# Optimization experiments

Measured on AMD Instinct MI355X. Metric: run time of the kernel, lower is better.

Reference implementation:

```python
import jax, jax.numpy as jnp
import numpy as np
from functools import partial

VOCAB = 1000
HID = 512
EPS = 1e-3  # Keras BatchNorm default epsilon


def _conv1d(x, w, stride):
    # x: [B,T,C_in], w: [K,C_in,C_out]
    return jax.lax.conv_general_dilated(x, w, window_strides=(stride,), padding='SAME',
                                        dimension_numbers=('NWC', 'WIO', 'NWC'))


def setup_inputs() -> dict:
    key = jax.random.key(0)
    ks = jax.random.split(key, 8)
    s = lambda *sh: 1.0 / np.sqrt(sh[-2] if len(sh) > 1 else sh[-1])
    return {
        'x': jax.random.normal(ks[0], (32, 1600, 80), jnp.float32),
        'y_true': jax.random.randint(ks[1], (32, 201), 0, VOCAB),
        'bn_gamma': jnp.ones((80,), jnp.float32),
        'bn_beta': jnp.zeros((80,), jnp.float32),
        'conv0_w': jax.random.normal(ks[2], (5, 80, 512), jnp.float32) * 0.05,
        'conv0_b': jnp.zeros((512,), jnp.float32),
        'tcr_w': jax.random.normal(ks[3], (4, 5, 512, 512), jnp.float32) * 0.02,
        'tcr_b': jnp.zeros((4, 512), jnp.float32),
        'gru_kernel': jax.random.normal(ks[4], (VOCAB, 3 * HID), jnp.float32) * 0.03,
        'gru_rec_kernel': jax.random.normal(ks[5], (HID, 3 * HID), jnp.float32) * 0.04,
        'gru_bias': jnp.zeros((2, 3 * HID), jnp.float32),
        'fc_w': jax.random.normal(ks[6], (2 * HID, VOCAB), jnp.float32) * 0.03,
        'fc_b': jnp.zeros((VOCAB,), jnp.float32),
    }


def reference(x, y_true, bn_gamma, bn_beta, conv0_w, conv0_b, tcr_w, tcr_b,
              gru_kernel, gru_rec_kernel, gru_bias, fc_w, fc_b):
    # ---- Encoder ----
    # BatchNorm (training mode: batch statistics over batch & time)
    mean = jnp.mean(x, axis=(0, 1))
    var = jnp.var(x, axis=(0, 1))
    h = (x - mean) * jax.lax.rsqrt(var + EPS) * bn_gamma + bn_beta
    # strided Conv1D + relu -> [B, T=800, 512]
    h = jax.nn.relu(_conv1d(h, conv0_w, 2) + conv0_b)
    # Temporal conv residual blocks: out = relu(conv(x)) + x
    for i in range(tcr_w.shape[0]):
        h = jax.nn.relu(_conv1d(h, tcr_w[i], 1) + tcr_b[i]) + h
    enc = h  # [B, T, D]
    B = enc.shape[0]

    # ---- Decoder (teacher forcing, training branch) ----
    y_oh = jax.nn.one_hot(y_true, VOCAB, dtype=jnp.float32)  # [B, U+1, V]
    inputs = jnp.transpose(y_oh[:, :-1, :], (1, 0, 2))       # [U, B, V]
    bi, br = gru_bias[0], gru_bias[1]

    def step(hstate, y_u):
        # Keras GRUCell (reset_after=True)
        mx = y_u @ gru_kernel + bi
        mh = hstate @ gru_rec_kernel + br
        xz, xr, xh = jnp.split(mx, 3, axis=-1)
        hz, hr, hh = jnp.split(mh, 3, axis=-1)
        z = jax.nn.sigmoid(xz + hz)
        r = jax.nn.sigmoid(xr + hr)
        cand = jnp.tanh(xh + r * hh)
        h_new = z * hstate + (1.0 - z) * cand
        # Dot-product attention over encoder states
        scores = jnp.einsum('bd,btd->bt', h_new, enc)
        alpha = jax.nn.softmax(scores, axis=-1)
        ctx = jnp.einsum('bt,btd->bd', alpha, enc)
        # output projection with softmax activation
        y_pred = jax.nn.softmax(jnp.concatenate([h_new, ctx], axis=1) @ fc_w + fc_b, axis=-1)
        return h_new, y_pred

    h0 = jnp.zeros((B, HID), jnp.float32)
    _, outs = jax.lax.scan(step, h0, inputs)  # [U, B, V]
    return jnp.transpose(outs, (1, 0, 2))     # [B, U, V]
```

## Files before the change

### kernel.cpp

```cpp
#include <hip/hip_runtime.h>
#include <cstdint>

typedef _Float16 f16;
typedef __attribute__((ext_vector_type(2))) _Float16 f16x2;
typedef __attribute__((ext_vector_type(8))) _Float16 f16x8;
typedef __attribute__((ext_vector_type(4))) float f32x4;
typedef __attribute__((ext_vector_type(2))) float f32x2;
typedef __attribute__((ext_vector_type(8))) unsigned short us8;
typedef __attribute__((ext_vector_type(4))) int i32x4;

#define NB   32
#define TIN  1600
#define CIN  80
#define TOUT 800
#define DH   512
#define NV   1000
#define NU   200
#define TXP  1604
#define THP  804
#define EPSB 1e-3f
#define EWG  248

__device__ __forceinline__ void st_sys_f16(f16* p, float v)
{
    f16 h = (f16)v;
    short s; __builtin_memcpy(&s, &h, 2);
    int si = (int)s;
    asm volatile("global_store_short %0, %1, off sc0 sc1"
                 :: "v"(p), "v"(si) : "memory");
}
__device__ __forceinline__ void st_sys_i32(int* p, int v)
{
    asm volatile("global_store_dword %0, %1, off sc0 sc1"
                 :: "v"(p), "v"(v) : "memory");
}

__device__ __forceinline__ void poll8(const int* fl, int target)
{
    i32x4 a, b;
    while (true) {
        asm volatile("global_load_dwordx4 %0, %2, off sc1\n\t"
                     "global_load_dwordx4 %1, %3, off sc1\n\t"
                     "s_waitcnt vmcnt(0)"
                     : "=&v"(a), "=&v"(b)
                     : "v"(fl), "v"(fl + 4)
                     : "memory");
        if (a.x == target && a.y == target && a.z == target && a.w == target &&
            b.x == target && b.y == target && b.z == target && b.w == target) break;
        __builtin_amdgcn_s_sleep(1);
    }
}

__device__ __forceinline__ float fast_tanh(float x)
{
    return 1.f - 2.f / (__expf(2.f * x) + 1.f);
}

__global__ void init_zero(float* gsum, float* gsumsq,
                          int* flags, int* lcnt, f16* xpad, f16* hbufA, f16* hbufB)
{
    int tid = blockIdx.x * 256 + threadIdx.x;
    int stride = gridDim.x * 256;
    if (blockIdx.x == 0) {
        if (threadIdx.x < 80) { gsum[threadIdx.x] = 0.f; gsumsq[threadIdx.x] = 0.f; }
        if (threadIdx.x >= 128 && threadIdx.x < 136) lcnt[threadIdx.x - 128] = 0;
    }
    for (int i = tid; i < NU * 8; i += stride) flags[i] = 0;
    for (int i = tid; i < NB * 4 * CIN; i += stride) {
        int b = i / (4 * CIN), rr = (i / CIN) % 4, c = i % CIN;
        int row = (rr == 0) ? 0 : (1600 + rr);
        xpad[((long)b * TXP + row) * CIN + c] = (f16)0.f;
    }
    for (int i = tid; i < 2 * NB * 4 * DH; i += stride) {
        int q = i; int buf = q / (NB * 4 * DH); q %= NB * 4 * DH;
        int b = q / (4 * DH); int rr = (q / DH) % 4; int dd = q % DH;
        int row = (rr < 2) ? rr : (800 + rr);
        f16* hb = buf ? hbufB : hbufA;
        hb[((long)b * THP + row) * DH + dd] = (f16)0.f;
    }
}

__global__ void transpose_f32_f16(const float* __restrict__ in, int R, int C,
                                  f16* __restrict__ out, int outRows, int outCols)
{
    __shared__ float t[32][33];
    int c0 = blockIdx.x * 32, r0 = blockIdx.y * 32;
    int x = threadIdx.x & 31, y = threadIdx.x >> 5;
    for (int i = y; i < 32; i += 8) {
        int r = r0 + i, c = c0 + x;
        t[i][x] = (r < R && c < C) ? in[(long)r * C + c] : 0.0f;
    }
    __syncthreads();
    for (int i = y; i < 32; i += 8) {
        int orow = c0 + i, ocol = r0 + x;
        if (orow < outRows && ocol < outCols)
            out[(long)orow * outCols + ocol] = (f16)t[x][i];
    }
}

__global__ void bn_stats(const float* __restrict__ x, float* gsum, float* gsumsq)
{
    __shared__ float ls[240], ls2[240];
    const float* base = x + (long)blockIdx.x * 200 * CIN;
    int tid = threadIdx.x;
    if (tid < 240) {
        int c = tid % 80, rg = tid / 80;
        float s = 0.f, s2 = 0.f;
        for (int r = rg; r < 200; r += 3) {
            float v = base[r * CIN + c];
            s += v; s2 += v * v;
        }
        ls[tid] = s; ls2[tid] = s2;
    }
    __syncthreads();
    if (tid < 80) {
        atomicAdd(&gsum[tid],   ls[tid] + ls[tid + 80] + ls[tid + 160]);
        atomicAdd(&gsumsq[tid], ls2[tid] + ls2[tid + 80] + ls2[tid + 160]);
    }
}

__global__ void bn_apply(const float* __restrict__ x, const float* __restrict__ gsum,
                         const float* __restrict__ gsumsq, const float* __restrict__ gamma,
                         const float* __restrict__ beta, f16* __restrict__ xpad)
{
    long idx = (long)blockIdx.x * 256 + threadIdx.x;
    if (idx >= (long)NB * TIN * CIN) return;
    int c = (int)(idx % CIN);
    long bt = idx / CIN;
    int t = (int)(bt % TIN); int b = (int)(bt / TIN);
    float mean = gsum[c] * (1.f / 51200.f);
    float var  = gsumsq[c] * (1.f / 51200.f) - mean * mean;
    float sc = gamma[c] * rsqrtf(var + EPSB);
    float sh = beta[c] - mean * sc;
    xpad[((long)b * TXP + t + 1) * CIN + c] = (f16)(x[idx] * sc + sh);
}

template<int MODE>
__launch_bounds__(256)
__global__ void gemm16(const f16* __restrict__ Ab, long strideA, long slabA,
                       const f16* __restrict__ Bb, long strideB, long slabB,
                       int M, int N, int Kchunks,
                       const float* __restrict__ bias,
                       float* __restrict__ outF)
{
    __shared__ f16 As[64][72];
    __shared__ f16 Bs[128][72];
    const int b = blockIdx.z;
    const f16* Abase = Ab + (long)b * slabA;
    const f16* Bbase = Bb + (long)b * slabB;
    const int m0 = blockIdx.x * 64, n0 = blockIdx.y * 128;
    const int tid = threadIdx.x;
    const int lane = tid & 63, wv = tid >> 6;
    const int lm = lane & 15, lk = lane >> 4;

    f32x4 vzero = {0.f, 0.f, 0.f, 0.f};
    f32x4 acc[4][2];
#pragma unroll
    for (int i = 0; i < 4; i++) { acc[i][0] = vzero; acc[i][1] = vzero; }

    const int srow = tid >> 3, scol = (tid & 7) * 8;

    for (int kc = 0; kc < Kchunks; kc++) {
        int kb = kc * 64;
#pragma unroll
        for (int p = 0; p < 2; p++) {
            int r = srow + p * 32;
            int m = m0 + r; if (m > M - 1) m = M - 1;
            *(us8*)&As[r][scol] = *(const us8*)(Abase + (long)m * strideA + kb + scol);
        }
#pragma unroll
        for (int p = 0; p < 4; p++) {
            int r = srow + p * 32;
            int n = n0 + r; if (n > N - 1) n = N - 1;
            *(us8*)&Bs[r][scol] = *(const us8*)(Bbase + (long)n * strideB + kb + scol);
        }
        __syncthreads();
#pragma unroll
        for (int ks = 0; ks < 2; ks++) {
            f16x8 af[4], bf[2];
#pragma unroll
            for (int mt = 0; mt < 4; mt++)
                af[mt] = *(const f16x8*)&As[mt * 16 + lm][ks * 32 + lk * 8];
#pragma unroll
            for (int nt = 0; nt < 2; nt++)
                bf[nt] = *(const f16x8*)&Bs[wv * 32 + nt * 16 + lm][ks * 32 + lk * 8];
#pragma unroll
            for (int mt = 0; mt < 4; mt++)
#pragma unroll
                for (int nt = 0; nt < 2; nt++)
                    acc[mt][nt] = __builtin_amdgcn_mfma_f32_16x16x32_f16(af[mt], bf[nt], acc[mt][nt], 0, 0, 0);
        }
        __syncthreads();
    }
#pragma unroll
    for (int mt = 0; mt < 4; mt++) {
#pragma unroll
        for (int nt = 0; nt < 2; nt++) {
            int n = n0 + wv * 32 + nt * 16 + lm;
#pragma unroll
            for (int reg = 0; reg < 4; reg++) {
                int m = m0 + mt * 16 + lk * 4 + reg;
                if (m >= M || n >= N) continue;
                float v = acc[mt][nt][reg];
                if (MODE == 2) {
                    outF[((long)b * NU + m) * 800 + n] = v;
                } else {
                    v += bias[n];
                    int u = m >> 5, bb = m & 31;
                    outF[((long)bb * NU + u) * 1000 + n] = v;
                }
            }
        }
    }
}

__device__ void enc_layer(int eb, int tid,
                          const f16* __restrict__ Ab, long strideA, long slabA,
                          const f16* __restrict__ Bb, long strideB,
                          int Kchunks, const float* __restrict__ bias,
                          const f16* __restrict__ resid, f16* __restrict__ outH,
                          long slabRO, f16 As[][72], f16 Bs[][72])
{
    const int lane = tid & 63, wv = tid >> 6;
    const int lm = lane & 15, lk = lane >> 4;
    const int srow = tid >> 3, scol = (tid & 7) * 8;
    f32x4 vzero = {0.f, 0.f, 0.f, 0.f};

    for (int t = eb; t < 1664; t += EWG) {
        int b = t / 52, rem = t - b * 52;
        int m0 = (rem >> 2) * 64, n0 = (rem & 3) * 128;
        const f16* Abase = Ab + (long)b * slabA;

        f32x4 acc[4][2];
#pragma unroll
        for (int i = 0; i < 4; i++) { acc[i][0] = vzero; acc[i][1] = vzero; }

        for (int kc = 0; kc < Kchunks; kc++) {
            int kb = kc * 64;
#pragma unroll
            for (int p = 0; p < 2; p++) {
                int r = srow + p * 32;
                int m = m0 + r; if (m > 799) m = 799;
                *(us8*)&As[r][scol] = *(const us8*)(Abase + (long)m * strideA + kb + scol);
            }
#pragma unroll
            for (int p = 0; p < 4; p++) {
                int r = srow + p * 32;
                *(us8*)&Bs[r][scol] = *(const us8*)(Bb + (long)(n0 + r) * strideB + kb + scol);
            }
            __syncthreads();
#pragma unroll
            for (int ks = 0; ks < 2; ks++) {
                f16x8 af[4], bf[2];
#pragma unroll
                for (int mt = 0; mt < 4; mt++)
                    af[mt] = *(const f16x8*)&As[mt * 16 + lm][ks * 32 + lk * 8];
#pragma unroll
                for (int nt = 0; nt < 2; nt++)
                    bf[nt] = *(const f16x8*)&Bs[wv * 32 + nt * 16 + lm][ks * 32 + lk * 8];
#pragma unroll
                for (int mt = 0; mt < 4; mt++)
#pragma unroll
                    for (int nt = 0; nt < 2; nt++)
                        acc[mt][nt] = __builtin_amdgcn_mfma_f32_16x16x32_f16(af[mt], bf[nt], acc[mt][nt], 0, 0, 0);
            }
            __syncthreads();
        }
#pragma unroll
        for (int mt = 0; mt < 4; mt++) {
#pragma unroll
            for (int nt = 0; nt < 2; nt++) {
                int n = n0 + wv * 32 + nt * 16 + lm;
#pragma unroll
                for (int reg = 0; reg < 4; reg++) {
                    int m = m0 + mt * 16 + lk * 4 + reg;
                    if (m >= 800) continue;
                    float v = acc[mt][nt][reg] + bias[n];
                    v = v > 0.f ? v : 0.f;
                    if (resid) v += (float)resid[(long)b * slabRO + (long)(2 + m) * DH + n];
                    outH[(long)b * slabRO + (long)(2 + m) * DH + n] = (f16)v;
                }
            }
        }
    }
}

__launch_bounds__(256, 1)
__global__ void enc_gru(const f16* __restrict__ wrecT, const float* __restrict__ gk,
                        const float* __restrict__ gbias, const int* __restrict__ ytrue,
                        f16* __restrict__ Hc, int* __restrict__ flags,
                        const f16* __restrict__ xpad, const f16* __restrict__ w0T,
                        const float* __restrict__ b0, const f16* __restrict__ tcrT,
                        const float* __restrict__ tcrb,
                        f16* __restrict__ hbufA, f16* __restrict__ hbufB,
                        int* __restrict__ lcnt)
{
    const int tid = threadIdx.x;

    if (blockIdx.x < 8) {
        __shared__ int yl[NU * 32];
        const int lane = tid & 63, wv = tid >> 6;
        const int gw = (int)blockIdx.x * 4 + wv;
        const int lm = lane & 15, lk = lane >> 4;
        const int j = gw * 16 + lm;

        for (int i = tid; i < NU * 32; i += 256) {
            int b = i / NU, u = i - b * NU;
            yl[u * 32 + b] = ytrue[b * 201 + u];
        }

        f16x8 wf[3][16];
#pragma unroll
        for (int g = 0; g < 3; g++)
#pragma unroll
            for (int ks = 0; ks < 16; ks++)
                wf[g][ks] = *(const f16x8*)&wrecT[(long)(g * 512 + j) * 512 + ks * 32 + lk * 8];

        const float biz = gbias[j],        bir = gbias[512 + j],        bic = gbias[1024 + j];
        const float brz = gbias[1536 + j], brr = gbias[1536 + 512 + j], brc = gbias[1536 + 1024 + j];
        f32x4 vzero = {0.f, 0.f, 0.f, 0.f};

        __syncthreads();

        float hold[8];
        float nxz[8], nxr[8], nxh[8], mxz[8], mxr[8], mxh[8];
#pragma unroll
        for (int s = 0; s < 8; s++) {
            hold[s] = 0.f;
            int b = ((s >> 2) << 4) + lk * 4 + (s & 3);
            const float* gkr = gk + (long)yl[b] * 1536;
            nxz[s] = gkr[j]; nxr[s] = gkr[512 + j]; nxh[s] = gkr[1024 + j];
        }

        for (int u = 0; u < NU; u++) {
            int up = (u < NU - 1) ? u + 1 : u;
#pragma unroll
            for (int s = 0; s < 8; s++) {
                int b = ((s >> 2) << 4) + lk * 4 + (s & 3);
                const float* gkr = gk + (long)yl[up * 32 + b] * 1536;
                mxz[s] = gkr[j]; mxr[s] = gkr[512 + j]; mxh[s] = gkr[1024 + j];
            }

            f32x4 acc[3][2];
#pragma unroll
            for (int g = 0; g < 3; g++) { acc[g][0] = vzero; acc[g][1] = vzero; }

            if (u > 0) {
                poll8(flags + (u - 1) * 8, u);
                const f16* hrow = Hc + (long)(u - 1) * 32 * 1024 + lk * 8;
#pragma unroll
                for (int ks = 0; ks < 16; ks++) {
                    f16x8 a0 = *(const f16x8*)(hrow + (long)lm * 1024 + ks * 32);
                    f16x8 a1 = *(const f16x8*)(hrow + (long)(16 + lm) * 1024 + ks * 32);
#pragma unroll
                    for (int g = 0; g < 3; g++) {
                        acc[g][0] = __builtin_amdgcn_mfma_f32_16x16x32_f16(a0, wf[g][ks], acc[g][0], 0, 0, 0);
                        acc[g][1] = __builtin_amdgcn_mfma_f32_16x16x32_f16(a1, wf[g][ks], acc[g][1], 0, 0, 0);
                    }
                }
            }

#pragma unroll
            for (int mt = 0; mt < 2; mt++) {
#pragma unroll
                for (int reg = 0; reg < 4; reg++) {
                    int s = mt * 4 + reg;
                    int b = mt * 16 + lk * 4 + reg;
                    float hz = acc[0][mt][reg] + brz;
                    float hr = acc[1][mt][reg] + brr;
                    float hh = acc[2][mt][reg] + brc;
                    float z = 1.f / (1.f + __expf(-(nxz[s] + biz + hz)));
                    float r = 1.f / (1.f + __expf(-(nxr[s] + bir + hr)));
                    float cd = fast_tanh(nxh[s] + bic + r * hh);
                    float hnew = z * hold[s] + (1.f - z) * cd;
                    hold[s] = hnew;
                    st_sys_f16(&Hc[((long)u * 32 + b) * 1024 + j], hnew);
                }
            }
#pragma unroll
            for (int s = 0; s < 8; s++) { nxz[s] = mxz[s]; nxr[s] = mxr[s]; nxh[s] = mxh[s]; }

            if (u < NU - 1) {
                asm volatile("s_waitcnt vmcnt(0)" ::: "memory");
                __syncthreads();
                if (tid == 0) st_sys_i32(&flags[u * 8 + (int)blockIdx.x], u + 1);
            }
        }
        asm volatile("s_waitcnt vmcnt(0)" ::: "memory");
        return;
    }

    __shared__ f16 As[64][72];
    __shared__ f16 Bs[128][72];
    const int eb = (int)blockIdx.x - 8;

    enc_layer(eb, tid, xpad, 160, (long)TXP * CIN, w0T, 448, 7, b0,
              nullptr, hbufA, (long)THP * DH, As, Bs);

    const f16* tin = hbufA; f16* tout = hbufB;
    for (int L = 0; L < 4; L++) {
        __syncthreads();
        if (tid == 0) {
            __hip_atomic_fetch_add(&lcnt[L], 1, __ATOMIC_RELEASE, __HIP_MEMORY_SCOPE_AGENT);
            while (__hip_atomic_load(&lcnt[L], __ATOMIC_RELAXED, __HIP_MEMORY_SCOPE_AGENT) < EWG)
                __builtin_amdgcn_s_sleep(8);
            (void)__hip_atomic_load(&lcnt[L], __ATOMIC_ACQUIRE, __HIP_MEMORY_SCOPE_AGENT);
        }
        __syncthreads();

        enc_layer(eb, tid, tin, 512, (long)THP * DH, tcrT + (size_t)L * 512 * 2560, 2560,
                  40, tcrb + L * 512, tin, tout, (long)THP * DH, As, Bs);
        const f16* t2 = tout; tout = (f16*)tin; tin = t2;
    }
}

__global__ void row_softmax(float* __restrict__ base, int len)
{
    float* s = base + (long)blockIdx.x * len;
    int tid = threadIdx.x;
    float v[4]; float mx = -1e30f;
#pragma unroll
    for (int i = 0; i < 4; i++) {
        int idx = tid + i * 256;
        v[i] = (idx < len) ? s[idx] : -1e30f;
        mx = fmaxf(mx, v[i]);
    }
#pragma unroll
    for (int off = 32; off; off >>= 1) mx = fmaxf(mx, __shfl_xor(mx, off));
    __shared__ float red[4], red2[4];
    if ((tid & 63) == 0) red[tid >> 6] = mx;
    __syncthreads();
    mx = fmaxf(fmaxf(red[0], red[1]), fmaxf(red[2], red[3]));
    float sum = 0.f;
#pragma unroll
    for (int i = 0; i < 4; i++) { v[i] = __expf(v[i] - mx); sum += v[i]; }
#pragma unroll
    for (int off = 32; off; off >>= 1) sum += __shfl_xor(sum, off);
    if ((tid & 63) == 0) red2[tid >> 6] = sum;
    __syncthreads();
    sum = red2[0] + red2[1] + red2[2] + red2[3];
    float inv = 1.f / sum;
#pragma unroll
    for (int i = 0; i < 4; i++) {
        int idx = tid + i * 256;
        if (idx < len) s[idx] = v[i] * inv;
    }
}

__global__ void ctx_kernel(const float* __restrict__ alpha, const f16* __restrict__ enc,
                           f16* __restrict__ Hc)
{
    __shared__ float al[800][18];
    int b = blockIdx.x, ut = blockIdx.y;
    int u0 = ut * 16;
    int tid = threadIdx.x;
    for (int ul = 0; ul < 16; ul++) {
        int u = u0 + ul;
        if (u < NU) {
            const float* arow = alpha + ((long)b * NU + u) * 800;
            for (int t = tid; t < 800; t += 256) al[t][ul] = arow[t];
        } else {
            for (int t = tid; t < 800; t += 256) al[t][ul] = 0.f;
        }
    }
    __syncthreads();
    int d0 = tid * 2;
    float a0[16], a1[16];
#pragma unroll
    for (int i = 0; i < 16; i++) { a0[i] = 0.f; a1[i] = 0.f; }
    const f16* encb = enc + ((long)b * THP + 2) * DH + d0;
    for (int t = 0; t < 800; t++) {
        f16x2 e = *(const f16x2*)&encb[(long)t * DH];
        float f0 = (float)e.x, f1 = (float)e.y;
#pragma unroll
        for (int g = 0; g < 8; g++) {
            f32x2 ap = *(const f32x2*)&al[t][2 * g];
            a0[2 * g]     += ap.x * f0; a0[2 * g + 1] += ap.y * f0;
            a1[2 * g]     += ap.x * f1; a1[2 * g + 1] += ap.y * f1;
        }
    }
#pragma unroll
    for (int ul = 0; ul < 16; ul++) {
        int u = u0 + ul;
        if (u < NU) {
            Hc[((long)u * 32 + b) * 1024 + 512 + d0]     = (f16)a0[ul];
            Hc[((long)u * 32 + b) * 1024 + 512 + d0 + 1] = (f16)a1[ul];
        }
    }
}

extern "C" void kernel_launch(void* const* d_in, const int* in_sizes, int n_in,
                              void* d_out, int out_size, void* d_ws, size_t ws_size,
                              hipStream_t stream)
{
    const float* x     = (const float*)d_in[0];
    const int*   ytrue = (const int*)d_in[1];
    const float* gamma = (const float*)d_in[2];
    const float* beta  = (const float*)d_in[3];
    const float* w0    = (const float*)d_in[4];
    const float* b0    = (const float*)d_in[5];
    const float* tcrw  = (const float*)d_in[6];
    const float* tcrb  = (const float*)d_in[7];
    const float* gk    = (const float*)d_in[8];
    const float* grk   = (const float*)d_in[9];
    const float* gbias = (const float*)d_in[10];
    const float* fcw   = (const float*)d_in[11];
    const float* fcb   = (const float*)d_in[12];
    float* out = (float*)d_out;
    (void)in_sizes; (void)n_in; (void)out_size; (void)ws_size;

    char* ws = (char*)d_ws;
    size_t o = 0;
    auto alloc = [&](size_t bytes) { size_t r = o; o += (bytes + 255) & ~(size_t)255; return r; };
    f16*   xpad   = (f16*)(ws + alloc((size_t)NB * TXP * CIN * 2));
    f16*   hbufA  = (f16*)(ws + alloc((size_t)NB * THP * DH * 2));
    f16*   hbufB  = (f16*)(ws + alloc((size_t)NB * THP * DH * 2));
    f16*   Hc     = (f16*)(ws + alloc((size_t)NU * NB * 1024 * 2));
    float* scores = (float*)(ws + alloc((size_t)NB * NU * 800 * 4));
    f16*   w0T    = (f16*)(ws + alloc((size_t)512 * 448 * 2));
    f16*   tcrT   = (f16*)(ws + alloc((size_t)4 * 512 * 2560 * 2));
    f16*   wrecT  = (f16*)(ws + alloc((size_t)1536 * 512 * 2));
    f16*   fcT    = (f16*)(ws + alloc((size_t)1024 * 1024 * 2));
    float* gsum   = (float*)(ws + alloc(80 * 4));
    float* gsumsq = (float*)(ws + alloc(80 * 4));
    int*   flags  = (int*)(ws + alloc(NU * 8 * 4));
    int*   lcnt   = (int*)(ws + alloc(64));

    init_zero<<<64, 256, 0, stream>>>(gsum, gsumsq, flags, lcnt, xpad, hbufA, hbufB);
    transpose_f32_f16<<<dim3(16, 14), 256, 0, stream>>>(w0, 400, 512, w0T, 512, 448);
    for (int i = 0; i < 4; i++)
        transpose_f32_f16<<<dim3(16, 80), 256, 0, stream>>>(tcrw + (size_t)i * 2560 * 512, 2560, 512,
                                                            tcrT + (size_t)i * 512 * 2560, 512, 2560);
    transpose_f32_f16<<<dim3(48, 16), 256, 0, stream>>>(grk, 512, 1536, wrecT, 1536, 512);
    transpose_f32_f16<<<dim3(32, 32), 256, 0, stream>>>(fcw, 1024, 1000, fcT, 1024, 1024);

    bn_stats<<<256, 256, 0, stream>>>(x, gsum, gsumsq);
    bn_apply<<<16000, 256, 0, stream>>>(x, gsum, gsumsq, gamma, beta, xpad);

    enc_gru<<<8 + EWG, 256, 0, stream>>>(wrecT, gk, gbias, ytrue, Hc, flags,
                                         xpad, w0T, b0, tcrT, tcrb, hbufA, hbufB, lcnt);
    const f16* enc = hbufA;

    gemm16<2><<<dim3(4, 7, 32), 256, 0, stream>>>(Hc, 32 * 1024, 1024, enc + 2 * DH, 512, (long)THP * DH,
        200, 800, 8, nullptr, scores);
    row_softmax<<<6400, 256, 0, stream>>>(scores, 800);
    ctx_kernel<<<dim3(32, 13), 256, 0, stream>>>(scores, enc, Hc);

    gemm16<3><<<dim3(100, 8, 1), 256, 0, stream>>>(Hc, 1024, 0, fcT, 1024, 0,
        6400, 1000, 16, fcb, out);
    row_softmax<<<6400, 256, 0, stream>>>(out, 1000);
}
```

Measured before the change: 1.860 ms.

## Fuse attention and output projection into persistent kernel, overlapped with GRU recurrence

The separate score GEMM, softmax, context kernel and FC GEMM are replaced by tasks run inside the persistent encoder/GRU kernel. Once the encoder finishes, worker blocks poll per-timestep GRU flags and compute attention in blocks of 8 timesteps, so this work overlaps with the serial recurrence. Each block publishes a completion flag that FC-projection tasks wait on. This removes several launches and the round trip of the scores buffer through global memory. The cost is more spin-polling, a more complex flag protocol, and shared-memory aliasing between task types.

```diff
diff --git a/kernel.cpp b/kernel.cpp
--- a/kernel.cpp
+++ b/kernel.cpp
@@ -12,7 +12,6 @@
 #define NB   32
 #define TIN  1600
 #define CIN  80
-#define TOUT 800
 #define DH   512
 #define NV   1000
 #define NU   200
@@ -20,19 +19,21 @@
 #define THP  804
 #define EPSB 1e-3f
 #define EWG  248
+#define UBLK 25
 
 __device__ __forceinline__ void st_sys_f16(f16* p, float v)
 {
-    f16 h = (f16)v;
-    short s; __builtin_memcpy(&s, &h, 2);
-    int si = (int)s;
-    asm volatile("global_store_short %0, %1, off sc0 sc1"
-                 :: "v"(p), "v"(si) : "memory");
+    f16 h = (f16)v; short s; __builtin_memcpy(&s, &h, 2); int si = (int)s;
+    asm volatile("global_store_short %0, %1, off sc0 sc1" :: "v"(p), "v"(si) : "memory");
+}
+__device__ __forceinline__ void st_sys_f16x2(f16* p, float a, float b)
+{
+    f16x2 h; h.x = (f16)a; h.y = (f16)b; int v; __builtin_memcpy(&v, &h, 4);
+    asm volatile("global_store_dword %0, %1, off sc0 sc1" :: "v"(p), "v"(v) : "memory");
 }
 __device__ __forceinline__ void st_sys_i32(int* p, int v)
 {
-    asm volatile("global_store_dword %0, %1, off sc0 sc1"
-                 :: "v"(p), "v"(v) : "memory");
+    asm volatile("global_store_dword %0, %1, off sc0 sc1" :: "v"(p), "v"(v) : "memory");
 }
 
 __device__ __forceinline__ void poll8(const int* fl, int target)
@@ -42,9 +43,7 @@
         asm volatile("global_load_dwordx4 %0, %2, off sc1\n\t"
                      "global_load_dwordx4 %1, %3, off sc1\n\t"
                      "s_waitcnt vmcnt(0)"
-                     : "=&v"(a), "=&v"(b)
-                     : "v"(fl), "v"(fl + 4)
-                     : "memory");
+                     : "=&v"(a), "=&v"(b) : "v"(fl), "v"(fl + 4) : "memory");
         if (a.x == target && a.y == target && a.z == target && a.w == target &&
             b.x == target && b.y == target && b.z == target && b.w == target) break;
         __builtin_amdgcn_s_sleep(1);
@@ -56,8 +55,20 @@
     return 1.f - 2.f / (__expf(2.f * x) + 1.f);
 }
 
-__global__ void init_zero(float* gsum, float* gsumsq,
-                          int* flags, int* lcnt, f16* xpad, f16* hbufA, f16* hbufB)
+__device__ __forceinline__ void wbar(int* slot)
+{
+    __syncthreads();
+    if (threadIdx.x == 0) {
+        __hip_atomic_fetch_add(slot, 1, __ATOMIC_RELEASE, __HIP_MEMORY_SCOPE_AGENT);
+        while (__hip_atomic_load(slot, __ATOMIC_RELAXED, __HIP_MEMORY_SCOPE_AGENT) < EWG)
+            __builtin_amdgcn_s_sleep(8);
+        (void)__hip_atomic_load(slot, __ATOMIC_ACQUIRE, __HIP_MEMORY_SCOPE_AGENT);
+    }
+    __syncthreads();
+}
+
+__global__ void init_zero(float* gsum, float* gsumsq, int* flags, int* cflag,
+                          int* lcnt, f16* xpad, f16* hbufA, f16* hbufB)
 {
     int tid = blockIdx.x * 256 + threadIdx.x;
     int stride = gridDim.x * 256;
@@ -66,6 +77,7 @@
         if (threadIdx.x >= 128 && threadIdx.x < 136) lcnt[threadIdx.x - 128] = 0;
     }
     for (int i = tid; i < NU * 8; i += stride) flags[i] = 0;
+    for (int i = tid; i < UBLK * 32; i += stride) cflag[i] = 0;
     for (int i = tid; i < NB * 4 * CIN; i += stride) {
         int b = i / (4 * CIN), rr = (i / CIN) % 4, c = i % CIN;
         int row = (rr == 0) ? 0 : (1600 + rr);
@@ -135,91 +147,12 @@
     xpad[((long)b * TXP + t + 1) * CIN + c] = (f16)(x[idx] * sc + sh);
 }
 
-template<int MODE>
-__launch_bounds__(256)
-__global__ void gemm16(const f16* __restrict__ Ab, long strideA, long slabA,
-                       const f16* __restrict__ Bb, long strideB, long slabB,
-                       int M, int N, int Kchunks,
-                       const float* __restrict__ bias,
-                       float* __restrict__ outF)
-{
-    __shared__ f16 As[64][72];
-    __shared__ f16 Bs[128][72];
-    const int b = blockIdx.z;
-    const f16* Abase = Ab + (long)b * slabA;
-    const f16* Bbase = Bb + (long)b * slabB;
-    const int m0 = blockIdx.x * 64, n0 = blockIdx.y * 128;
-    const int tid = threadIdx.x;
-    const int lane = tid & 63, wv = tid >> 6;
-    const int lm = lane & 15, lk = lane >> 4;
-
-    f32x4 vzero = {0.f, 0.f, 0.f, 0.f};
-    f32x4 acc[4][2];
-#pragma unroll
-    for (int i = 0; i < 4; i++) { acc[i][0] = vzero; acc[i][1] = vzero; }
-
-    const int srow = tid >> 3, scol = (tid & 7) * 8;
-
-    for (int kc = 0; kc < Kchunks; kc++) {
-        int kb = kc * 64;
-#pragma unroll
-        for (int p = 0; p < 2; p++) {
-            int r = srow + p * 32;
-            int m = m0 + r; if (m > M - 1) m = M - 1;
-            *(us8*)&As[r][scol] = *(const us8*)(Abase + (long)m * strideA + kb + scol);
-        }
-#pragma unroll
-        for (int p = 0; p < 4; p++) {
-            int r = srow + p * 32;
-            int n = n0 + r; if (n > N - 1) n = N - 1;
-            *(us8*)&Bs[r][scol] = *(const us8*)(Bbase + (long)n * strideB + kb + scol);
-        }
-        __syncthreads();
-#pragma unroll
-        for (int ks = 0; ks < 2; ks++) {
-            f16x8 af[4], bf[2];
-#pragma unroll
-            for (int mt = 0; mt < 4; mt++)
-                af[mt] = *(const f16x8*)&As[mt * 16 + lm][ks * 32 + lk * 8];
-#pragma unroll
-            for (int nt = 0; nt < 2; nt++)
-                bf[nt] = *(const f16x8*)&Bs[wv * 32 + nt * 16 + lm][ks * 32 + lk * 8];
-#pragma unroll
-            for (int mt = 0; mt < 4; mt++)
-#pragma unroll
-                for (int nt = 0; nt < 2; nt++)
-                    acc[mt][nt] = __builtin_amdgcn_mfma_f32_16x16x32_f16(af[mt], bf[nt], acc[mt][nt], 0, 0, 0);
-        }
-        __syncthreads();
-    }
-#pragma unroll
-    for (int mt = 0; mt < 4; mt++) {
-#pragma unroll
-        for (int nt = 0; nt < 2; nt++) {
-            int n = n0 + wv * 32 + nt * 16 + lm;
-#pragma unroll
-            for (int reg = 0; reg < 4; reg++) {
-                int m = m0 + mt * 16 + lk * 4 + reg;
-                if (m >= M || n >= N) continue;
-                float v = acc[mt][nt][reg];
-                if (MODE == 2) {
-                    outF[((long)b * NU + m) * 800 + n] = v;
-                } else {
-                    v += bias[n];
-                    int u = m >> 5, bb = m & 31;
-                    outF[((long)bb * NU + u) * 1000 + n] = v;
-                }
-            }
-        }
-    }
-}
-
 __device__ void enc_layer(int eb, int tid,
                           const f16* __restrict__ Ab, long strideA, long slabA,
                           const f16* __restrict__ Bb, long strideB,
                           int Kchunks, const float* __restrict__ bias,
                           const f16* __restrict__ resid, f16* __restrict__ outH,
-                          long slabRO, f16 As[][72], f16 Bs[][72])
+                          long slabRO, f16 (*As)[72], f16 (*Bs)[72])
 {
     const int lane = tid & 63, wv = tid >> 6;
     const int lm = lane & 15, lk = lane >> 4;
@@ -285,15 +218,164 @@
     }
 }
 
+__device__ void task1(int k, int b, int tid, const f16* __restrict__ Hc_c,
+                      f16* __restrict__ Hc, const f16* __restrict__ encb,
+                      const int* __restrict__ flags, int* __restrict__ cflag,
+                      f16 (*hA)[512], float (*sc)[808])
+{
+    const int lane = tid & 63, wv = tid >> 6;
+    const int lm = lane & 15, lk = lane >> 4;
+
+    poll8(flags + (8 * k + 7) * 8, 8 * k + 8);
+
+    for (int c = tid; c < 512; c += 256) {
+        int u = c >> 6, d = (c & 63) * 8;
+        *(us8*)&hA[u][d] = *(const us8*)(Hc_c + ((long)(8 * k + u) * 32 + b) * 1024 + d);
+    }
+    __syncthreads();
+
+    f16x8 af[16];
+#pragma unroll
+    for (int ks = 0; ks < 16; ks++)
+        af[ks] = *(const f16x8*)&hA[lm & 7][ks * 32 + lk * 8];
+
+    for (int tt = wv; tt < 50; tt += 4) {
+        f32x4 acc = {0.f, 0.f, 0.f, 0.f};
+        const f16* bb = encb + (long)(tt * 16 + lm) * DH + lk * 8;
+#pragma unroll
+        for (int ks = 0; ks < 16; ks++) {
+            f16x8 bf = *(const f16x8*)(bb + ks * 32);
+            acc = __builtin_amdgcn_mfma_f32_16x16x32_f16(af[ks], bf, acc, 0, 0, 0);
+        }
+#pragma unroll
+        for (int reg = 0; reg < 4; reg++) {
+            int row = lk * 4 + reg;
+            if (row < 8) sc[row][tt * 16 + lm] = acc[reg];
+        }
+    }
+    __syncthreads();
+
+    for (int rr = wv; rr < 8; rr += 4) {
+        float mx = -1e30f;
+        for (int i = lane; i < 800; i += 64) mx = fmaxf(mx, sc[rr][i]);
+#pragma unroll
+        for (int off = 32; off; off >>= 1) mx = fmaxf(mx, __shfl_xor(mx, off));
+        float sum = 0.f;
+        for (int i = lane; i < 800; i += 64) {
+            float e = __expf(sc[rr][i] - mx);
+            sc[rr][i] = e; sum += e;
+        }
+#pragma unroll
+        for (int off = 32; off; off >>= 1) sum += __shfl_xor(sum, off);
+        float inv = 1.f / sum;
+        for (int i = lane; i < 800; i += 64) sc[rr][i] *= inv;
+    }
+    __syncthreads();
+
+    int d0 = tid * 2;
+    float c0[8], c1[8];
+#pragma unroll
+    for (int u = 0; u < 8; u++) { c0[u] = 0.f; c1[u] = 0.f; }
+    const f16* ep = encb + d0;
+    for (int t = 0; t < 800; t++) {
+        f16x2 e = *(const f16x2*)(ep + (long)t * DH);
+        float f0 = (float)e.x, f1 = (float)e.y;
+#pragma unroll
+        for (int u = 0; u < 8; u++) {
+            float a = sc[u][t];
+            c0[u] += a * f0; c1[u] += a * f1;
+        }
+    }
+#pragma unroll
+    for (int u = 0; u < 8; u++)
+        st_sys_f16x2(&Hc[((long)(8 * k + u) * 32 + b) * 1024 + 512 + d0], c0[u], c1[u]);
+
+    asm volatile("s_waitcnt vmcnt(0)" ::: "memory");
+    __syncthreads();
+    if (tid == 0) st_sys_i32(&cflag[k * 32 + b], 1);
+}
+
+__device__ void task2(int k, int v, int tid, const f16* __restrict__ Hc_c,
+                      const f16* __restrict__ fcT, const float* __restrict__ fcb,
+                      float* __restrict__ out, const int* __restrict__ cflag,
+                      f16 (*As)[72], f16 (*Bs)[72])
+{
+    const int lane = tid & 63, wv = tid >> 6;
+    const int lm = lane & 15, lk = lane >> 4;
+    const int srow = tid >> 3, scol = (tid & 7) * 8;
+    const int n0 = v * 128;
+    const f16* Abase = Hc_c + (long)k * 256 * 1024;
+    f32x4 vzero = {0.f, 0.f, 0.f, 0.f};
+
+    poll8(cflag + k * 32,      1);
+    poll8(cflag + k * 32 + 8,  1);
+    poll8(cflag + k * 32 + 16, 1);
+    poll8(cflag + k * 32 + 24, 1);
+    __syncthreads();
+
+    for (int mt4 = 0; mt4 < 4; mt4++) {
+        int m0 = mt4 * 64;
+        f32x4 acc[4][2];
+#pragma unroll
+        for (int i = 0; i < 4; i++) { acc[i][0] = vzero; acc[i][1] = vzero; }
+
+        for (int kc = 0; kc < 16; kc++) {
+            int kb = kc * 64;
+#pragma unroll
+            for (int p = 0; p < 2; p++) {
+                int r = srow + p * 32;
+                *(us8*)&As[r][scol] = *(const us8*)(Abase + (long)(m0 + r) * 1024 + kb + scol);
+            }
+#pragma unroll
+            for (int p = 0; p < 4; p++) {
+                int r = srow + p * 32;
+                *(us8*)&Bs[r][scol] = *(const us8*)(fcT + (long)(n0 + r) * 1024 + kb + scol);
+            }
+            __syncthreads();
+#pragma unroll
+            for (int ks = 0; ks < 2; ks++) {
+                f16x8 af[4], bf[2];
+#pragma unroll
+                for (int mt = 0; mt < 4; mt++)
+                    af[mt] = *(const f16x8*)&As[mt * 16 + lm][ks * 32 + lk * 8];
+#pragma unroll
+                for (int nt = 0; nt < 2; nt++)
+                    bf[nt] = *(const f16x8*)&Bs[wv * 32 + nt * 16 + lm][ks * 32 + lk * 8];
+#pragma unroll
+                for (int mt = 0; mt < 4; mt++)
+#pragma unroll
+                    for (int nt = 0; nt < 2; nt++)
+                        acc[mt][nt] = __builtin_amdgcn_mfma_f32_16x16x32_f16(af[mt], bf[nt], acc[mt][nt], 0, 0, 0);
+            }
+            __syncthreads();
+        }
+#pragma unroll
+        for (int mt = 0; mt < 4; mt++) {
+#pragma unroll
+            for (int nt = 0; nt < 2; nt++) {
+                int n = n0 + wv * 32 + nt * 16 + lm;
+                if (n >= NV) continue;
+#pragma unroll
+                for (int reg = 0; reg < 4; reg++) {
+                    int m = m0 + mt * 16 + lk * 4 + reg;
+                    int u = 8 * k + (m >> 5), b = m & 31;
+                    out[((long)b * NU + u) * 1000 + n] = acc[mt][nt][reg] + fcb[n];
+                }
+            }
+        }
+    }
+}
+
 __launch_bounds__(256, 1)
 __global__ void enc_gru(const f16* __restrict__ wrecT, const float* __restrict__ gk,
                         const float* __restrict__ gbias, const int* __restrict__ ytrue,
-                        f16* __restrict__ Hc, int* __restrict__ flags,
+                        f16* __restrict__ Hc, int* __restrict__ flags, int* __restrict__ cflag,
                         const f16* __restrict__ xpad, const f16* __restrict__ w0T,
                         const float* __restrict__ b0, const f16* __restrict__ tcrT,
                         const float* __restrict__ tcrb,
                         f16* __restrict__ hbufA, f16* __restrict__ hbufB,
-                        int* __restrict__ lcnt)
+                        const f16* __restrict__ fcT, const float* __restrict__ fcb,
+                        float* __restrict__ out, int* __restrict__ lcnt)
 {
     const int tid = threadIdx.x;
 
@@ -380,18 +462,20 @@
 #pragma unroll
             for (int s = 0; s < 8; s++) { nxz[s] = mxz[s]; nxr[s] = mxr[s]; nxh[s] = mxh[s]; }
 
-            if (u < NU - 1) {
-                asm volatile("s_waitcnt vmcnt(0)" ::: "memory");
-                __syncthreads();
-                if (tid == 0) st_sys_i32(&flags[u * 8 + (int)blockIdx.x], u + 1);
-            }
+            asm volatile("s_waitcnt vmcnt(0)" ::: "memory");
+            __syncthreads();
+            if (tid == 0) st_sys_i32(&flags[u * 8 + (int)blockIdx.x], u + 1);
         }
         asm volatile("s_waitcnt vmcnt(0)" ::: "memory");
         return;
     }
 
-    __shared__ f16 As[64][72];
-    __shared__ f16 Bs[128][72];
+    __shared__ char smraw[34048] __attribute__((aligned(16)));
+    f16 (*As)[72]   = (f16(*)[72])smraw;
+    f16 (*Bs)[72]   = (f16(*)[72])(smraw + 9216);
+    f16 (*hA)[512]  = (f16(*)[512])smraw;
+    float (*sc)[808]= (float(*)[808])(smraw + 8192);
+
     const int eb = (int)blockIdx.x - 8;
 
     enc_layer(eb, tid, xpad, 160, (long)TXP * CIN, w0T, 448, 7, b0,
@@ -399,18 +483,22 @@
 
     const f16* tin = hbufA; f16* tout = hbufB;
     for (int L = 0; L < 4; L++) {
-        __syncthreads();
-        if (tid == 0) {
-            __hip_atomic_fetch_add(&lcnt[L], 1, __ATOMIC_RELEASE, __HIP_MEMORY_SCOPE_AGENT);
-            while (__hip_atomic_load(&lcnt[L], __ATOMIC_RELAXED, __HIP_MEMORY_SCOPE_AGENT) < EWG)
-                __builtin_amdgcn_s_sleep(8);
-            (void)__hip_atomic_load(&lcnt[L], __ATOMIC_ACQUIRE, __HIP_MEMORY_SCOPE_AGENT);
-        }
-        __syncthreads();
-
+        wbar(&lcnt[L]);
         enc_layer(eb, tid, tin, 512, (long)THP * DH, tcrT + (size_t)L * 512 * 2560, 2560,
                   40, tcrb + L * 512, tin, tout, (long)THP * DH, As, Bs);
         const f16* t2 = tout; tout = (f16*)tin; tin = t2;
+    }
+    wbar(&lcnt[4]);
+    const f16* encA = hbufA;
+
+    for (int t = eb; t < UBLK * 40; t += EWG) {
+        int k = t / 40, r = t - k * 40;
+        if (r < 32) {
+            task1(k, r, tid, Hc, Hc, encA + ((long)r * THP + 2) * DH, flags, cflag, hA, sc);
+        } else {
+            task2(k, r - 32, tid, Hc, fcT, fcb, out, cflag, As, Bs);
+        }
+        __syncthreads();
     }
 }
 
@@ -444,48 +532,6 @@
     for (int i = 0; i < 4; i++) {
         int idx = tid + i * 256;
         if (idx < len) s[idx] = v[i] * inv;
-    }
-}
-
-__global__ void ctx_kernel(const float* __restrict__ alpha, const f16* __restrict__ enc,
-                           f16* __restrict__ Hc)
-{
-    __shared__ float al[800][18];
-    int b = blockIdx.x, ut = blockIdx.y;
-    int u0 = ut * 16;
-    int tid = threadIdx.x;
-    for (int ul = 0; ul < 16; ul++) {
-        int u = u0 + ul;
-        if (u < NU) {
-            const float* arow = alpha + ((long)b * NU + u) * 800;
-            for (int t = tid; t < 800; t += 256) al[t][ul] = arow[t];
-        } else {
-            for (int t = tid; t < 800; t += 256) al[t][ul] = 0.f;
-        }
-    }
-    __syncthreads();
-    int d0 = tid * 2;
-    float a0[16], a1[16];
-#pragma unroll
-    for (int i = 0; i < 16; i++) { a0[i] = 0.f; a1[i] = 0.f; }
-    const f16* encb = enc + ((long)b * THP + 2) * DH + d0;
-    for (int t = 0; t < 800; t++) {
-        f16x2 e = *(const f16x2*)&encb[(long)t * DH];
-        float f0 = (float)e.x, f1 = (float)e.y;
-#pragma unroll
-        for (int g = 0; g < 8; g++) {
-            f32x2 ap = *(const f32x2*)&al[t][2 * g];
-            a0[2 * g]     += ap.x * f0; a0[2 * g + 1] += ap.y * f0;
-            a1[2 * g]     += ap.x * f1; a1[2 * g + 1] += ap.y * f1;
-        }
-    }
-#pragma unroll
-    for (int ul = 0; ul < 16; ul++) {
-        int u = u0 + ul;
-        if (u < NU) {
-            Hc[((long)u * 32 + b) * 1024 + 512 + d0]     = (f16)a0[ul];
-            Hc[((long)u * 32 + b) * 1024 + 512 + d0 + 1] = (f16)a1[ul];
-        }
     }
 }
 
@@ -516,7 +562,6 @@
     f16*   hbufA  = (f16*)(ws + alloc((size_t)NB * THP * DH * 2));
     f16*   hbufB  = (f16*)(ws + alloc((size_t)NB * THP * DH * 2));
     f16*   Hc     = (f16*)(ws + alloc((size_t)NU * NB * 1024 * 2));
-    float* scores = (float*)(ws + alloc((size_t)NB * NU * 800 * 4));
     f16*   w0T    = (f16*)(ws + alloc((size_t)512 * 448 * 2));
     f16*   tcrT   = (f16*)(ws + alloc((size_t)4 * 512 * 2560 * 2));
     f16*   wrecT  = (f16*)(ws + alloc((size_t)1536 * 512 * 2));
@@ -524,9 +569,10 @@
     float* gsum   = (float*)(ws + alloc(80 * 4));
     float* gsumsq = (float*)(ws + alloc(80 * 4));
     int*   flags  = (int*)(ws + alloc(NU * 8 * 4));
+    int*   cflag  = (int*)(ws + alloc(UBLK * 32 * 4));
     int*   lcnt   = (int*)(ws + alloc(64));
 
-    init_zero<<<64, 256, 0, stream>>>(gsum, gsumsq, flags, lcnt, xpad, hbufA, hbufB);
+    init_zero<<<64, 256, 0, stream>>>(gsum, gsumsq, flags, cflag, lcnt, xpad, hbufA, hbufB);
     transpose_f32_f16<<<dim3(16, 14), 256, 0, stream>>>(w0, 400, 512, w0T, 512, 448);
     for (int i = 0; i < 4; i++)
         transpose_f32_f16<<<dim3(16, 80), 256, 0, stream>>>(tcrw + (size_t)i * 2560 * 512, 2560, 512,
@@ -537,16 +583,9 @@
     bn_stats<<<256, 256, 0, stream>>>(x, gsum, gsumsq);
     bn_apply<<<16000, 256, 0, stream>>>(x, gsum, gsumsq, gamma, beta, xpad);
 
-    enc_gru<<<8 + EWG, 256, 0, stream>>>(wrecT, gk, gbias, ytrue, Hc, flags,
-                                         xpad, w0T, b0, tcrT, tcrb, hbufA, hbufB, lcnt);
-    const f16* enc = hbufA;
-
-    gemm16<2><<<dim3(4, 7, 32), 256, 0, stream>>>(Hc, 32 * 1024, 1024, enc + 2 * DH, 512, (long)THP * DH,
-        200, 800, 8, nullptr, scores);
-    row_softmax<<<6400, 256, 0, stream>>>(scores, 800);
-    ctx_kernel<<<dim3(32, 13), 256, 0, stream>>>(scores, enc, Hc);
-
-    gemm16<3><<<dim3(100, 8, 1), 256, 0, stream>>>(Hc, 1024, 0, fcT, 1024, 0,
-        6400, 1000, 16, fcb, out);
+    enc_gru<<<8 + EWG, 256, 0, stream>>>(wrecT, gk, gbias, ytrue, Hc, flags, cflag,
+                                         xpad, w0T, b0, tcrT, tcrb, hbufA, hbufB,
+                                         fcT, fcb, out, lcnt);
+
     row_softmax<<<6400, 256, 0, stream>>>(out, 1000);
 }
```

Result: slower. 1.992 ms (+7.1%).
